# Kernel optimization log

Measured on AMD Instinct MI355X. Metric: run time of the kernel, lower is better.

## Reference

```python
import jax, jax.numpy as jnp
import numpy as np

TAU = 0.1
LAMBD = 0.75
EPS = 1e-8  # torch cosine_similarity norm clamp


def setup_inputs() -> dict:
    key = jax.random.key(0)
    k1, k2 = jax.random.split(key)
    B, D = 8192, 768
    v = jax.random.normal(k1, (B, D), dtype=jnp.float32)
    u = jax.random.normal(k2, (B, D), dtype=jnp.float32)
    return {"v": v, "u": u}


def reference(v, u):
    # Batched equivalent of the per-sample Python loop:
    # cos(v_i, u_j) = <v_i/||v_i||, u_j/||u_j||>, with torch's eps clamp on norms.
    v = v.astype(jnp.float32)
    u = u.astype(jnp.float32)
    vn = v / jnp.maximum(jnp.linalg.norm(v, axis=1, keepdims=True), EPS)
    un = u / jnp.maximum(jnp.linalg.norm(u, axis=1, keepdims=True), EPS)
    sim = jnp.einsum('id,jd->ij', vn, un) / TAU  # [B, B] logits
    diag = jnp.diagonal(sim)
    # image->text: -log( exp(sim_ii) / sum_j exp(sim_ij) )
    loss_it = jax.nn.logsumexp(sim, axis=1) - diag
    # text->image: -log( exp(sim_ii) / sum_j exp(sim_ji) )
    loss_ti = jax.nn.logsumexp(sim, axis=0) - diag
    # In the torch source text_image calls .item(), detaching it from autograd.
    loss_ti = jax.lax.stop_gradient(loss_ti)
    return jnp.mean(LAMBD * loss_it + (1.0 - LAMBD) * loss_ti)
```

## Files before the change

kernel.cpp:

```cpp
#include <hip/hip_runtime.h>
#include <hip/hip_bf16.h>

typedef unsigned char u8;
typedef unsigned short u16;
typedef unsigned int u32;
typedef float f32x16 __attribute__((ext_vector_type(16)));
typedef float f32x2 __attribute__((ext_vector_type(2)));
typedef int i32x4 __attribute__((ext_vector_type(4)));
typedef int i32x8 __attribute__((ext_vector_type(8)));

#define B_SZ 8192
#define D_SZ 768
#define TAU_INV 10.0f
#define ESCALE 0.014088818758681283f
#define FP4_SCALE 32.0f
#define SCHRAU_K1 118185.58f
#define SCHRAU_K2 1064879685.0f


__device__ __forceinline__ u32 fp4_enc(float x) {
    float y = fabsf(x);
    u32 n = (u32)(y >= 0.25f) + (u32)(y >= 0.75f) + (u32)(y >= 1.25f) +
            (u32)(y >= 1.75f) + (u32)(y >= 2.5f)  + (u32)(y >= 3.5f) +
            (u32)(y >= 5.0f);
    return n | (x < 0.f ? 8u : 0u);
}

__device__ __forceinline__ u16 fp4_pack4(float x, float y, float z, float w) {
    return (u16)(fp4_enc(x) | (fp4_enc(y) << 4) | (fp4_enc(z) << 8) | (fp4_enc(w) << 12));
}

__global__ __launch_bounds__(256) void norm_kernel(const float4* __restrict__ v,
                                                   const float4* __restrict__ u,
                                                   u16* __restrict__ vn,
                                                   u16* __restrict__ un,
                                                   float* __restrict__ diag) {
    const int wid = threadIdx.x >> 6, lane = threadIdx.x & 63;
    const int row = blockIdx.x * 4 + wid;
    const float4* vr = v + (size_t)row * 192;
    const float4* ur = u + (size_t)row * 192;
    float4 a[3], b[3];
    float sv = 0.f, su = 0.f, sd = 0.f;
#pragma unroll
    for (int c = 0; c < 3; ++c) {
        a[c] = vr[lane + 64 * c];
        b[c] = ur[lane + 64 * c];
        sv += a[c].x * a[c].x + a[c].y * a[c].y + a[c].z * a[c].z + a[c].w * a[c].w;
        su += b[c].x * b[c].x + b[c].y * b[c].y + b[c].z * b[c].z + b[c].w * b[c].w;
        sd += a[c].x * b[c].x + a[c].y * b[c].y + a[c].z * b[c].z + a[c].w * b[c].w;
    }
#pragma unroll
    for (int m = 1; m < 64; m <<= 1) {
        sv += __shfl_xor(sv, m);
        su += __shfl_xor(su, m);
        sd += __shfl_xor(sd, m);
    }
    const float iv = FP4_SCALE / fmaxf(sqrtf(sv), 1e-8f);
    const float iu = FP4_SCALE / fmaxf(sqrtf(su), 1e-8f);
    const int rg = row >> 5, rr = row & 31;
#pragma unroll
    for (int c = 0; c < 3; ++c) {
        u16 pa = fp4_pack4(a[c].x * iv, a[c].y * iv, a[c].z * iv, a[c].w * iv);
        u16 pb = fp4_pack4(b[c].x * iu, b[c].y * iu, b[c].z * iu, b[c].w * iu);
        const int e = lane + 64 * c;
        const int idx = (rg * 12 + (e >> 4)) * 512 + ((e >> 3) & 1) * 256 + rr * 8 + (e & 7);
        vn[idx] = pa;
        un[idx] = pb;
    }
    if (lane == 0) diag[row] = sd * iv * iu * TAU_INV / (FP4_SCALE * FP4_SCALE);
}

__device__ __forceinline__ i32x8 ldsfrag(const u8* p) {
    i32x4 lo = *(const i32x4*)p;
    return __builtin_shufflevector(lo, lo, 0, 1, 2, 3, -1, -1, -1, -1);
}

__device__ __forceinline__ void gload_lds16(const u8* g, u8* l) {
    __builtin_amdgcn_global_load_lds((const __attribute__((address_space(1))) void*)g,
                                     (__attribute__((address_space(3))) void*)l, 16, 0, 0);
}

__device__ __forceinline__ f32x16 mx_mfma4(i32x8 a, i32x8 b, f32x16 c) {
    return __builtin_amdgcn_mfma_scale_f32_32x32x64_f8f6f4(
        a, b, c, 4, 4, 0, 0x7F7F7F7F, 0, 0x7F7F7F7F);
}

__global__ __launch_bounds__(512, 2) void simexp_kernel(const u8* __restrict__ vn,
                                                        const u8* __restrict__ un,
                                                        float* __restrict__ rowP,
                                                        float* __restrict__ colP) {
    __shared__ __attribute__((aligned(16))) u8 stg[3][16][2][1024];
    __shared__ float rowLds[4][256];
    __shared__ float colLds[2][256];

    const int tid  = threadIdx.x;
    const int w    = tid >> 6;
    const int lane = tid & 63;
    const int l32  = lane & 31;
    const int h    = lane >> 5;
    const int wr = w >> 2, wc = w & 3;

    const int id = blockIdx.x;
    const int chunk = id >> 6;
    const int li = id & 63;
    const int rb = ((chunk >> 2) << 3) + (li >> 3);
    const int cb = ((chunk & 3) << 3) + (li & 7);

    const u8* gA = vn + (size_t)(rb * 8 + w) * 12288 + (u32)lane * 16;
    const u8* gB = un + (size_t)(cb * 8 + w) * 12288 + (u32)lane * 16;

    f32x16 acc[4][2];
#pragma unroll
    for (int i = 0; i < 4; ++i)
#pragma unroll
        for (int j = 0; j < 2; ++j)
#pragma unroll
            for (int r = 0; r < 16; ++r) acc[i][j][r] = 0.f;

#define STAGE(t)                                                  \
    {                                                             \
        gload_lds16(gA + (2 * (t)) * 1024,     &stg[(t) % 3][w][0][0]);     \
        gload_lds16(gA + (2 * (t) + 1) * 1024, &stg[(t) % 3][w][1][0]);     \
        gload_lds16(gB + (2 * (t)) * 1024,     &stg[(t) % 3][8 + w][0][0]); \
        gload_lds16(gB + (2 * (t) + 1) * 1024, &stg[(t) % 3][8 + w][1][0]); \
    }

    STAGE(0)
    STAGE(1)
    asm volatile("s_waitcnt vmcnt(4)\n\ts_barrier" ::: "memory");

#pragma unroll
    for (int t = 0; t < 6; ++t) {
        if (t + 2 < 6) STAGE(t + 2)
        const u8* s = &stg[t % 3][0][0][0] + (u32)lane * 16;
#pragma unroll
        for (int kk = 0; kk < 2; ++kk) {
            i32x8 fa0 = ldsfrag(s + ((wr * 4 + 0) * 2 + kk) * 1024);
            i32x8 fa1 = ldsfrag(s + ((wr * 4 + 1) * 2 + kk) * 1024);
            i32x8 fa2 = ldsfrag(s + ((wr * 4 + 2) * 2 + kk) * 1024);
            i32x8 fa3 = ldsfrag(s + ((wr * 4 + 3) * 2 + kk) * 1024);
            i32x8 fb0 = ldsfrag(s + ((8 + wc * 2 + 0) * 2 + kk) * 1024);
            i32x8 fb1 = ldsfrag(s + ((8 + wc * 2 + 1) * 2 + kk) * 1024);
            __builtin_amdgcn_s_setprio(1);
            acc[0][0] = mx_mfma4(fa0, fb0, acc[0][0]);
            acc[1][0] = mx_mfma4(fa1, fb0, acc[1][0]);
            acc[2][0] = mx_mfma4(fa2, fb0, acc[2][0]);
            acc[3][0] = mx_mfma4(fa3, fb0, acc[3][0]);
            acc[0][1] = mx_mfma4(fa0, fb1, acc[0][1]);
            acc[1][1] = mx_mfma4(fa1, fb1, acc[1][1]);
            acc[2][1] = mx_mfma4(fa2, fb1, acc[2][1]);
            acc[3][1] = mx_mfma4(fa3, fb1, acc[3][1]);
            __builtin_amdgcn_s_setprio(0);
        }
        if (t < 4)       asm volatile("s_waitcnt vmcnt(4)\n\ts_barrier" ::: "memory");
        else if (t == 4) asm volatile("s_waitcnt vmcnt(0)\n\ts_barrier" ::: "memory");
    }
#undef STAGE

    f32x2 va[16], vb[16];
    f32x2 cacc2[2];
#pragma unroll
    for (int p = 0; p < 16; ++p) {
        va[p].x = 0.f; va[p].y = 0.f;
        vb[p].x = 0.f; vb[p].y = 0.f;
    }
    cacc2[0].x = 0.f; cacc2[0].y = 0.f;
    cacc2[1].x = 0.f; cacc2[1].y = 0.f;
#pragma unroll
    for (int i = 0; i < 4; ++i)
#pragma unroll
        for (int j = 0; j < 2; ++j)
#pragma unroll
            for (int r = 0; r < 16; r += 2) {
                f32x2 a;
                a.x = acc[i][j][r];
                a.y = acc[i][j][r + 1];
                f32x2 t = a * SCHRAU_K1 + SCHRAU_K2;
                f32x2 e;
                e.x = __int_as_float((int)t.x);
                e.y = __int_as_float((int)t.y);
                if (i < 2) va[(i & 1) * 8 + (r >> 1)] += e;
                else       vb[(i & 1) * 8 + (r >> 1)] += e;
                cacc2[j] += e;
            }

#pragma unroll
    for (int m = 16; m >= 2; m >>= 1) {
        const int n = m >> 1;
        const bool hi = (l32 & m) != 0;
#pragma unroll
        for (int p = 0; p < n; ++p) {
            {
                f32x2 a = va[p], b = va[p + n];
                f32x2 x, y;
                x.x = hi ? b.x : a.x;  x.y = hi ? b.y : a.y;
                y.x = hi ? a.x : b.x;  y.y = hi ? a.y : b.y;
                f32x2 s;
                s.x = __shfl_xor(y.x, m);
                s.y = __shfl_xor(y.y, m);
                va[p] = x + s;
            }
            {
                f32x2 a = vb[p], b = vb[p + n];
                f32x2 x, y;
                x.x = hi ? b.x : a.x;  x.y = hi ? b.y : a.y;
                y.x = hi ? a.x : b.x;  y.y = hi ? a.y : b.y;
                f32x2 s;
                s.x = __shfl_xor(y.x, m);
                s.y = __shfl_xor(y.y, m);
                vb[p] = x + s;
            }
        }
    }
    {
        f32x2 s;
        s.x = __shfl_xor(va[0].x, 1);
        s.y = __shfl_xor(va[0].y, 1);
        va[0] += s;
        s.x = __shfl_xor(vb[0].x, 1);
        s.y = __shfl_xor(vb[0].y, 1);
        vb[0] += s;
    }
    {
        const int q = (l32 >> 1) & 15;
        const int tt = 2 * q + (l32 & 1);
        const int i2 = tt >> 4, r2 = tt & 15;
        const int rbase = i2 * 32 + (r2 & 3) + 8 * (r2 >> 2) + 4 * h;
        rowLds[wc][wr * 128 + rbase]      = (l32 & 1) ? va[0].y : va[0].x;
        rowLds[wc][wr * 128 + 64 + rbase] = (l32 & 1) ? vb[0].y : vb[0].x;
    }
    {
        float c0 = cacc2[0].x + cacc2[0].y;
        float c1 = cacc2[1].x + cacc2[1].y;
        c0 += __shfl_xor(c0, 32);
        c1 += __shfl_xor(c1, 32);
        if (h == 0) {
            colLds[wr][wc * 64 + l32]      = c0;
            colLds[wr][wc * 64 + 32 + l32] = c1;
        }
    }
    __syncthreads();
    if (tid < 256) {
        rowP[(size_t)cb * B_SZ + rb * 256 + tid] =
            rowLds[0][tid] + rowLds[1][tid] + rowLds[2][tid] + rowLds[3][tid];
    } else {
        const int t = tid - 256;
        colP[(size_t)rb * B_SZ + cb * 256 + t] = colLds[0][t] + colLds[1][t];
    }
}

__global__ __launch_bounds__(256) void finalize_kernel(const float* __restrict__ rowP,
                                                       const float* __restrict__ colP,
                                                       const float* __restrict__ diag,
                                                       float* __restrict__ out) {
    const int i = blockIdx.x * 256 + threadIdx.x;
    float rs = 0.f, cs = 0.f;
#pragma unroll 8
    for (int p = 0; p < 32; ++p) {
        rs += rowP[(size_t)p * B_SZ + i];
        cs += colP[(size_t)p * B_SZ + i];
    }
    float contrib = (0.75f * logf(rs) + 0.25f * logf(cs) - diag[i]) * (1.0f / (float)B_SZ);
#pragma unroll
    for (int m = 1; m < 64; m <<= 1) contrib += __shfl_xor(contrib, m);
    __shared__ float red[4];
    const int wid = threadIdx.x >> 6, lane = threadIdx.x & 63;
    if (lane == 0) red[wid] = contrib;
    __syncthreads();
    if (threadIdx.x == 0) atomicAdd(out, red[0] + red[1] + red[2] + red[3]);
}

extern "C" void kernel_launch(void* const* d_in, const int* in_sizes, int n_in,
                              void* d_out, int out_size, void* d_ws, size_t ws_size,
                              hipStream_t stream) {
    const float* v = (const float*)d_in[0];
    const float* u = (const float*)d_in[1];
    char* ws = (char*)d_ws;
    u16* vn4   = (u16*)(ws);
    u16* un4   = (u16*)(ws + 3145728);
    float* dg  = (float*)(ws + 6291456);
    float* rwp = (float*)(ws + 6324224);
    float* clp = (float*)(ws + 7372800);
    float* out = (float*)d_out;

    hipMemsetAsync(out, 0, sizeof(float), stream);
    hipLaunchKernelGGL(norm_kernel, dim3(2048), dim3(256), 0, stream,
                       (const float4*)v, (const float4*)u, vn4, un4, dg);
    hipLaunchKernelGGL(simexp_kernel, dim3(1024), dim3(512), 0, stream,
                       (const u8*)vn4, (const u8*)un4, rwp, clp);
    hipLaunchKernelGGL(finalize_kernel, dim3(B_SZ / 256), dim3(256), 0, stream, rwp, clp, dg, out);
}
```

Measured before the change: 129.2 us.

## Deepen LDS pipeline to four single-k stages and swizzle block order

Restructures the K loop from six steps of two k-slices with a 3-buffer ring into twelve single-slice steps with a 4-buffer ring and prefetch distance three. An extra barrier after the fragment loads lets the next stage's writes be issued earlier. Block indices are also remapped so consecutive workgroups are spread across chunks, which may change L2/XCD locality. The cost is more barriers per tile and a different cache-sharing pattern.

```diff
diff --git a/kernel.cpp b/kernel.cpp
--- a/kernel.cpp
+++ b/kernel.cpp
@@ -89,7 +89,7 @@
                                                         const u8* __restrict__ un,
                                                         float* __restrict__ rowP,
                                                         float* __restrict__ colP) {
-    __shared__ __attribute__((aligned(16))) u8 stg[3][16][2][1024];
+    __shared__ __attribute__((aligned(16))) u8 stg[4][16][1024];
     __shared__ float rowLds[4][256];
     __shared__ float colLds[2][256];
 
@@ -100,7 +100,8 @@
     const int h    = lane >> 5;
     const int wr = w >> 2, wc = w & 3;
 
-    const int id = blockIdx.x;
+    const int id0 = blockIdx.x;
+    const int id  = (id0 & 7) * 128 + (id0 >> 3);
     const int chunk = id >> 6;
     const int li = id & 63;
     const int rb = ((chunk >> 2) << 3) + (li >> 3);
@@ -117,43 +118,41 @@
 #pragma unroll
             for (int r = 0; r < 16; ++r) acc[i][j][r] = 0.f;
 
-#define STAGE(t)                                                  \
-    {                                                             \
-        gload_lds16(gA + (2 * (t)) * 1024,     &stg[(t) % 3][w][0][0]);     \
-        gload_lds16(gA + (2 * (t) + 1) * 1024, &stg[(t) % 3][w][1][0]);     \
-        gload_lds16(gB + (2 * (t)) * 1024,     &stg[(t) % 3][8 + w][0][0]); \
-        gload_lds16(gB + (2 * (t) + 1) * 1024, &stg[(t) % 3][8 + w][1][0]); \
+#define STAGE(t)                                              \
+    {                                                         \
+        gload_lds16(gA + (t) * 1024, &stg[(t) & 3][w][0]);    \
+        gload_lds16(gB + (t) * 1024, &stg[(t) & 3][8 + w][0]);\
     }
 
     STAGE(0)
     STAGE(1)
+    STAGE(2)
     asm volatile("s_waitcnt vmcnt(4)\n\ts_barrier" ::: "memory");
 
 #pragma unroll
-    for (int t = 0; t < 6; ++t) {
-        if (t + 2 < 6) STAGE(t + 2)
-        const u8* s = &stg[t % 3][0][0][0] + (u32)lane * 16;
-#pragma unroll
-        for (int kk = 0; kk < 2; ++kk) {
-            i32x8 fa0 = ldsfrag(s + ((wr * 4 + 0) * 2 + kk) * 1024);
-            i32x8 fa1 = ldsfrag(s + ((wr * 4 + 1) * 2 + kk) * 1024);
-            i32x8 fa2 = ldsfrag(s + ((wr * 4 + 2) * 2 + kk) * 1024);
-            i32x8 fa3 = ldsfrag(s + ((wr * 4 + 3) * 2 + kk) * 1024);
-            i32x8 fb0 = ldsfrag(s + ((8 + wc * 2 + 0) * 2 + kk) * 1024);
-            i32x8 fb1 = ldsfrag(s + ((8 + wc * 2 + 1) * 2 + kk) * 1024);
-            __builtin_amdgcn_s_setprio(1);
-            acc[0][0] = mx_mfma4(fa0, fb0, acc[0][0]);
-            acc[1][0] = mx_mfma4(fa1, fb0, acc[1][0]);
-            acc[2][0] = mx_mfma4(fa2, fb0, acc[2][0]);
-            acc[3][0] = mx_mfma4(fa3, fb0, acc[3][0]);
-            acc[0][1] = mx_mfma4(fa0, fb1, acc[0][1]);
-            acc[1][1] = mx_mfma4(fa1, fb1, acc[1][1]);
-            acc[2][1] = mx_mfma4(fa2, fb1, acc[2][1]);
-            acc[3][1] = mx_mfma4(fa3, fb1, acc[3][1]);
-            __builtin_amdgcn_s_setprio(0);
-        }
-        if (t < 4)       asm volatile("s_waitcnt vmcnt(4)\n\ts_barrier" ::: "memory");
-        else if (t == 4) asm volatile("s_waitcnt vmcnt(0)\n\ts_barrier" ::: "memory");
+    for (int t = 0; t < 12; ++t) {
+        if (t <= 8) STAGE(t + 3)
+        const u8* s = &stg[t & 3][0][0] + (u32)lane * 16;
+        i32x8 fa0 = ldsfrag(s + (wr * 4 + 0) * 1024);
+        i32x8 fa1 = ldsfrag(s + (wr * 4 + 1) * 1024);
+        i32x8 fa2 = ldsfrag(s + (wr * 4 + 2) * 1024);
+        i32x8 fa3 = ldsfrag(s + (wr * 4 + 3) * 1024);
+        i32x8 fb0 = ldsfrag(s + (8 + wc * 2 + 0) * 1024);
+        i32x8 fb1 = ldsfrag(s + (8 + wc * 2 + 1) * 1024);
+        asm volatile("s_barrier" ::: "memory");
+        __builtin_amdgcn_s_setprio(1);
+        acc[0][0] = mx_mfma4(fa0, fb0, acc[0][0]);
+        acc[1][0] = mx_mfma4(fa1, fb0, acc[1][0]);
+        acc[2][0] = mx_mfma4(fa2, fb0, acc[2][0]);
+        acc[3][0] = mx_mfma4(fa3, fb0, acc[3][0]);
+        acc[0][1] = mx_mfma4(fa0, fb1, acc[0][1]);
+        acc[1][1] = mx_mfma4(fa1, fb1, acc[1][1]);
+        acc[2][1] = mx_mfma4(fa2, fb1, acc[2][1]);
+        acc[3][1] = mx_mfma4(fa3, fb1, acc[3][1]);
+        __builtin_amdgcn_s_setprio(0);
+        if (t <= 8)       asm volatile("s_waitcnt vmcnt(4)\n\ts_barrier" ::: "memory");
+        else if (t == 9)  asm volatile("s_waitcnt vmcnt(2)\n\ts_barrier" ::: "memory");
+        else if (t == 10) asm volatile("s_waitcnt vmcnt(0)\n\ts_barrier" ::: "memory");
     }
 #undef STAGE
 
```

Result: no change. 129.4 us (+0.1%).
